# Performance work log

Hardware: AMD Instinct MI355X
Metric: run time of the kernel (lower is better)

## Reference

```python
import jax, jax.numpy as jnp
import numpy as np

N = 100000
E = 1600000
IN_DIM = 64
EMB_DIM = 64
BN_EPS = 1e-5


def setup_inputs() -> dict:
    key = jax.random.key(0)
    ks = jax.random.split(key, 8)
    x = jax.random.normal(ks[0], (N, IN_DIM), dtype=jnp.float32)
    edge_index = jax.random.randint(ks[1], (2, E), 0, N, dtype=jnp.int64)
    # GIN learned epsilon (train_eps=True), initialized to 0 as in PyG
    eps = jnp.zeros((), dtype=jnp.float32)
    # MLP params: Linear(in, emb) -> BN -> ReLU -> Linear(emb, emb)
    s1 = 1.0 / np.sqrt(IN_DIM)
    W1 = jax.random.uniform(ks[2], (IN_DIM, EMB_DIM), jnp.float32, -s1, s1)
    b1 = jax.random.uniform(ks[3], (EMB_DIM,), jnp.float32, -s1, s1)
    gamma = jnp.ones((EMB_DIM,), jnp.float32)
    beta = jnp.zeros((EMB_DIM,), jnp.float32)
    s2 = 1.0 / np.sqrt(EMB_DIM)
    W2 = jax.random.uniform(ks[4], (EMB_DIM, EMB_DIM), jnp.float32, -s2, s2)
    b2 = jax.random.uniform(ks[5], (EMB_DIM,), jnp.float32, -s2, s2)
    return {"x": x, "edge_index": edge_index, "eps": eps,
            "W1": W1, "b1": b1, "gamma": gamma, "beta": beta,
            "W2": W2, "b2": b2}


def reference(x, edge_index, eps, W1, b1, gamma, beta, W2, b2):
    src, dst = edge_index[0], edge_index[1]
    # GIN aggregation: sum of neighbor (source) features at each destination
    agg = jax.ops.segment_sum(x[src], dst, num_segments=N)  # [N, IN_DIM]
    h = (1.0 + eps) * x + agg
    # MLP: Linear -> BatchNorm1d (training-mode batch stats) -> ReLU -> Linear
    h1 = h @ W1 + b1                                   # [N, EMB_DIM]
    mean = jnp.mean(h1, axis=0)
    var = jnp.mean((h1 - mean) ** 2, axis=0)           # biased var, as torch BN
    h1n = (h1 - mean) * jax.lax.rsqrt(var + BN_EPS) * gamma + beta
    h2 = jax.nn.relu(h1n)
    return h2 @ W2 + b2                                # [N, EMB_DIM]
```

## Files before the change

### kernel.cpp

```cpp
#include <hip/hip_runtime.h>

#define NNODES 100000
#define NEDGES 1600000
#define DIM 64
#define NB 782
#define NPB 256
#define CHUNK 6250
#define CAP 3968
#define HP 68
#define NTILES 6250

typedef __attribute__((ext_vector_type(4))) float f32x4;
typedef __attribute__((ext_vector_type(8))) short s16x8;

__device__ __forceinline__ unsigned short bf16_rne(float f) {
  unsigned u = __float_as_uint(f);
  u += 0x7FFF + ((u >> 16) & 1);
  return (unsigned short)(u >> 16);
}
__device__ __forceinline__ float bf16_to_f32(unsigned short h) {
  return __uint_as_float(((unsigned)h) << 16);
}

__global__ __launch_bounds__(1024) void initpack_kernel(
    int* __restrict__ gcursor, float* __restrict__ sums,
    const float* __restrict__ W1, const float* __restrict__ W2,
    unsigned short* __restrict__ Wp1, unsigned short* __restrict__ Wp2) {
  int t = threadIdx.x;
  if (t < NB) gcursor[t] = t * CAP;
  if (t < 2 * DIM) sums[t] = 0.0f;
  if (t < 128) {
    int lane = t & 63;
    const float* W = (t >= 64) ? W2 : W1;
    unsigned short* Wp = (t >= 64) ? Wp2 : Wp1;
    int q = lane >> 4, n16 = lane & 15;
#pragma unroll
    for (int f = 0; f < 8; ++f) {
      int kk = f >> 2, nt = f & 3;
#pragma unroll
      for (int j = 0; j < 8; ++j) {
        int k = kk * 32 + q * 8 + j;
        int n = nt * 16 + n16;
        Wp[f * 512 + lane * 8 + j] = bf16_rne(W[k * DIM + n]);
      }
    }
  }
}

__global__ __launch_bounds__(256) void convert_kernel(
    const float* __restrict__ x, unsigned short* __restrict__ xb) {
  int i = blockIdx.x * 256 + threadIdx.x;
  float4 v = ((const float4*)x)[i];
  ushort4 o;
  o.x = bf16_rne(v.x); o.y = bf16_rne(v.y);
  o.z = bf16_rne(v.z); o.w = bf16_rne(v.w);
  ((ushort4*)xb)[i] = o;
}

__global__ __launch_bounds__(1024) void partition_kernel(
    const int* __restrict__ ei, int* __restrict__ gcursor,
    int* __restrict__ bpart) {
  __shared__ int lh[NB];
  __shared__ int cur[NB];
  int t = threadIdx.x;
  for (int b = t; b < NB; b += 1024) lh[b] = 0;
  __syncthreads();
  int base = blockIdx.x * CHUNK;
  for (int i = t; i < CHUNK; i += 1024)
    atomicAdd(&lh[ei[NEDGES + base + i] >> 7], 1);
  __syncthreads();
  for (int b = t; b < NB; b += 1024) {
    int c = lh[b];
    cur[b] = c ? atomicAdd(&gcursor[b], c) : 0;
  }
  __syncthreads();
  for (int i = t; i < CHUNK; i += 1024) {
    int s = ei[base + i];
    int d = ei[NEDGES + base + i];
    int p = atomicAdd(&cur[d >> 7], 1);
    bpart[p] = ((d & 127) << 17) | s;
  }
}

__global__ __launch_bounds__(512) void mega_kernel(
    const int* __restrict__ bpart, const int* __restrict__ gcursor,
    const unsigned short* __restrict__ xb, float* __restrict__ h1,
    const unsigned short* __restrict__ Wp, const float* __restrict__ b1,
    const float* __restrict__ epsp,
    float* __restrict__ sums, float* __restrict__ sumsq) {
  __shared__ int sd[128];
  __shared__ int cur[128];
  __shared__ int stage[CAP];
  __shared__ float hbuf[128 * HP];
  __shared__ float lsum[DIM];
  __shared__ float lsq[DIM];
  int b = blockIdx.x;
  int t = threadIdx.x;
  if (t < 128) sd[t] = 0;
  if (t < DIM) { lsum[t] = 0.0f; lsq[t] = 0.0f; }
  __syncthreads();
  int pbase = b * CAP;
  int cnt = gcursor[b] - pbase;
  for (int i = t; i < cnt; i += 512)
    atomicAdd(&sd[bpart[pbase + i] >> 17], 1);
  __syncthreads();
  int deg = (t < 128) ? sd[t] : 0;
  for (int off = 1; off < 128; off <<= 1) {
    int a = (t < 128 && t >= off) ? sd[t - off] : 0;
    __syncthreads();
    if (t < 128) sd[t] += a;
    __syncthreads();
  }
  if (t < 128) cur[t] = sd[t] - deg;
  __syncthreads();
  for (int i = t; i < cnt; i += 512) {
    int v = bpart[pbase + i];
    int p = atomicAdd(&cur[v >> 17], 1);
    stage[p] = v & 0x1FFFF;
  }
  __syncthreads();
  {
    int part = t & 15;
    int ng = t >> 4;
#pragma unroll 1
    for (int pass = 0; pass < 4; ++pass) {
      int nl = ng + pass * 32;
      int e0 = (nl == 0) ? 0 : sd[nl - 1];
      int e1 = sd[nl];
      float4 a0 = make_float4(0.f, 0.f, 0.f, 0.f);
      float4 a1 = a0, a2 = a0, a3 = a0;
      int e = e0;
      for (; e + 4 <= e1; e += 4) {
        int s0 = stage[e + 0];
        int s1 = stage[e + 1];
        int s2 = stage[e + 2];
        int s3 = stage[e + 3];
        ushort4 u0 = ((const ushort4*)(xb + (size_t)s0 * DIM))[part];
        ushort4 u1 = ((const ushort4*)(xb + (size_t)s1 * DIM))[part];
        ushort4 u2 = ((const ushort4*)(xb + (size_t)s2 * DIM))[part];
        ushort4 u3 = ((const ushort4*)(xb + (size_t)s3 * DIM))[part];
        a0.x += bf16_to_f32(u0.x); a0.y += bf16_to_f32(u0.y);
        a0.z += bf16_to_f32(u0.z); a0.w += bf16_to_f32(u0.w);
        a1.x += bf16_to_f32(u1.x); a1.y += bf16_to_f32(u1.y);
        a1.z += bf16_to_f32(u1.z); a1.w += bf16_to_f32(u1.w);
        a2.x += bf16_to_f32(u2.x); a2.y += bf16_to_f32(u2.y);
        a2.z += bf16_to_f32(u2.z); a2.w += bf16_to_f32(u2.w);
        a3.x += bf16_to_f32(u3.x); a3.y += bf16_to_f32(u3.y);
        a3.z += bf16_to_f32(u3.z); a3.w += bf16_to_f32(u3.w);
      }
      for (; e < e1; ++e) {
        int s = stage[e];
        ushort4 u = ((const ushort4*)(xb + (size_t)s * DIM))[part];
        a0.x += bf16_to_f32(u.x); a0.y += bf16_to_f32(u.y);
        a0.z += bf16_to_f32(u.z); a0.w += bf16_to_f32(u.w);
      }
      float4 acc;
      acc.x = (a0.x + a1.x) + (a2.x + a3.x);
      acc.y = (a0.y + a1.y) + (a2.y + a3.y);
      acc.z = (a0.z + a1.z) + (a2.z + a3.z);
      acc.w = (a0.w + a1.w) + (a2.w + a3.w);
      *(float4*)&hbuf[nl * HP + part * 4] = acc;
    }
  }
  __syncthreads();
  {
    int wave = t >> 6;
    int lane = t & 63;
    int tile = b * 8 + wave;
    if (tile < NTILES) {
      int q = lane >> 4;
      int r16 = lane & 15;
      float onep = 1.0f + epsp[0];
      s16x8 bf[8];
#pragma unroll
      for (int f = 0; f < 8; ++f)
        bf[f] = ((const s16x8*)Wp)[f * 64 + lane];
      int lrow = wave * 16 + r16;
      int grow = b * 128 + lrow;
      const s16x8* xrow = (const s16x8*)(xb + (size_t)grow * DIM);
      f32x4 acc[4] = {{0.f,0.f,0.f,0.f},{0.f,0.f,0.f,0.f},
                      {0.f,0.f,0.f,0.f},{0.f,0.f,0.f,0.f}};
#pragma unroll
      for (int kk = 0; kk < 2; ++kk) {
        s16x8 xv = xrow[kk * 4 + q];
        const float* hb = &hbuf[lrow * HP + kk * 32 + q * 8];
        float4 h0 = *(const float4*)hb;
        float4 h4 = *(const float4*)(hb + 4);
        s16x8 a;
        a[0] = (short)bf16_rne(fmaf(onep, bf16_to_f32((unsigned short)xv[0]), h0.x));
        a[1] = (short)bf16_rne(fmaf(onep, bf16_to_f32((unsigned short)xv[1]), h0.y));
        a[2] = (short)bf16_rne(fmaf(onep, bf16_to_f32((unsigned short)xv[2]), h0.z));
        a[3] = (short)bf16_rne(fmaf(onep, bf16_to_f32((unsigned short)xv[3]), h0.w));
        a[4] = (short)bf16_rne(fmaf(onep, bf16_to_f32((unsigned short)xv[4]), h4.x));
        a[5] = (short)bf16_rne(fmaf(onep, bf16_to_f32((unsigned short)xv[5]), h4.y));
        a[6] = (short)bf16_rne(fmaf(onep, bf16_to_f32((unsigned short)xv[6]), h4.z));
        a[7] = (short)bf16_rne(fmaf(onep, bf16_to_f32((unsigned short)xv[7]), h4.w));
#pragma unroll
        for (int nt = 0; nt < 4; ++nt)
          acc[nt] = __builtin_amdgcn_mfma_f32_16x16x32_bf16(
              a, bf[kk * 4 + nt], acc[nt], 0, 0, 0);
      }
      int orow = tile * 16 + q * 4;
#pragma unroll
      for (int nt = 0; nt < 4; ++nt) {
        int col = nt * 16 + r16;
        float bb = b1[col];
        float sl = 0.0f, ql = 0.0f;
#pragma unroll
        for (int r = 0; r < 4; ++r) {
          float v = acc[nt][r] + bb;
          h1[(size_t)(orow + r) * DIM + col] = v;
          sl += v;
          ql = fmaf(v, v, ql);
        }
        sl += __shfl_down(sl, 32); ql += __shfl_down(ql, 32);
        sl += __shfl_down(sl, 16); ql += __shfl_down(ql, 16);
        if (q == 0) {
          atomicAdd(&lsum[col], sl);
          atomicAdd(&lsq[col], ql);
        }
      }
    }
  }
  __syncthreads();
  if (t < DIM) {
    atomicAdd(&sums[t], lsum[t]);
    atomicAdd(&sumsq[t], lsq[t]);
  }
}

__global__ __launch_bounds__(256) void fused2_kernel(
    const float* __restrict__ h1, float* __restrict__ out,
    const unsigned short* __restrict__ Wp, const float* __restrict__ b2,
    const float* __restrict__ gamma, const float* __restrict__ beta,
    const float* __restrict__ sums, const float* __restrict__ sumsq) {
  __shared__ float sc_s[DIM];
  __shared__ float sh_s[DIM];
  int t = threadIdx.x;
  if (t < DIM) {
    float invN = 1.0f / (float)NNODES;
    float m = sums[t] * invN;
    float v = fmaf(-m, m, sumsq[t] * invN);
    float sc = gamma[t] * rsqrtf(v + 1e-5f);
    sc_s[t] = sc;
    sh_s[t] = fmaf(-m, sc, beta[t]);
  }
  __syncthreads();
  int wave = t >> 6;
  int lane = t & 63;
  int tile = blockIdx.x * 4 + wave;
  if (tile >= NTILES) return;
  int q = lane >> 4;
  int r16 = lane & 15;
  s16x8 bf[8];
#pragma unroll
  for (int f = 0; f < 8; ++f)
    bf[f] = ((const s16x8*)Wp)[f * 64 + lane];
  int arow = tile * 16 + r16;
  const float* hr = h1 + (size_t)arow * DIM + q * 8;
  f32x4 acc[4] = {{0.f,0.f,0.f,0.f},{0.f,0.f,0.f,0.f},
                  {0.f,0.f,0.f,0.f},{0.f,0.f,0.f,0.f}};
#pragma unroll
  for (int kk = 0; kk < 2; ++kk) {
    int kbase = kk * 32 + q * 8;
    float4 hv0 = *(const float4*)(hr + kk * 32);
    float4 hv1 = *(const float4*)(hr + kk * 32 + 4);
    float4 sc0 = *(const float4*)(sc_s + kbase);
    float4 sc1 = *(const float4*)(sc_s + kbase + 4);
    float4 sh0 = *(const float4*)(sh_s + kbase);
    float4 sh1 = *(const float4*)(sh_s + kbase + 4);
    s16x8 a;
    a[0] = (short)bf16_rne(fmaxf(fmaf(hv0.x, sc0.x, sh0.x), 0.f));
    a[1] = (short)bf16_rne(fmaxf(fmaf(hv0.y, sc0.y, sh0.y), 0.f));
    a[2] = (short)bf16_rne(fmaxf(fmaf(hv0.z, sc0.z, sh0.z), 0.f));
    a[3] = (short)bf16_rne(fmaxf(fmaf(hv0.w, sc0.w, sh0.w), 0.f));
    a[4] = (short)bf16_rne(fmaxf(fmaf(hv1.x, sc1.x, sh1.x), 0.f));
    a[5] = (short)bf16_rne(fmaxf(fmaf(hv1.y, sc1.y, sh1.y), 0.f));
    a[6] = (short)bf16_rne(fmaxf(fmaf(hv1.z, sc1.z, sh1.z), 0.f));
    a[7] = (short)bf16_rne(fmaxf(fmaf(hv1.w, sc1.w, sh1.w), 0.f));
#pragma unroll
    for (int nt = 0; nt < 4; ++nt)
      acc[nt] = __builtin_amdgcn_mfma_f32_16x16x32_bf16(
          a, bf[kk * 4 + nt], acc[nt], 0, 0, 0);
  }
  int orow = tile * 16 + q * 4;
#pragma unroll
  for (int nt = 0; nt < 4; ++nt) {
    int col = nt * 16 + r16;
    float bb = b2[col];
#pragma unroll
    for (int r = 0; r < 4; ++r)
      out[(size_t)(orow + r) * DIM + col] = acc[nt][r] + bb;
  }
}

extern "C" void kernel_launch(void* const* d_in, const int* in_sizes, int n_in,
                              void* d_out, int out_size, void* d_ws, size_t ws_size,
                              hipStream_t stream) {
  (void)in_sizes; (void)n_in; (void)out_size; (void)ws_size;
  const float* x     = (const float*)d_in[0];
  const int*   ei    = (const int*)d_in[1];
  const float* eps   = (const float*)d_in[2];
  const float* W1    = (const float*)d_in[3];
  const float* b1    = (const float*)d_in[4];
  const float* gamma = (const float*)d_in[5];
  const float* beta  = (const float*)d_in[6];
  const float* W2    = (const float*)d_in[7];
  const float* b2    = (const float*)d_in[8];
  float* outp = (float*)d_out;

  const int N = NNODES;

  float* h1      = (float*)d_ws;
  float* sums    = h1 + (size_t)N * DIM;
  float* sumsq   = sums + DIM;
  int*   gcursor = (int*)(sumsq + DIM);
  unsigned short* Wp1 = (unsigned short*)(gcursor + ((NB + 1) & ~1));
  unsigned short* Wp2 = Wp1 + 4096;
  int*            bpart = (int*)d_out;
  unsigned short* xb    = (unsigned short*)d_out + (size_t)NB * CAP * 2;

  initpack_kernel <<<1, 1024, 0, stream>>>(gcursor, sums, W1, W2, Wp1, Wp2);
  convert_kernel  <<<N * DIM / 4 / 256, 256, 0, stream>>>(x, xb);
  partition_kernel<<<NPB, 1024, 0, stream>>>(ei, gcursor, bpart);
  mega_kernel     <<<NB, 512, 0, stream>>>(bpart, gcursor, xb, h1,
                                           Wp1, b1, eps, sums, sumsq);
  fused2_kernel   <<<(NTILES + 3) / 4, 256, 0, stream>>>(h1, outp, Wp2, b2,
                                                         gamma, beta, sums, sumsq);
}
```

Measured before the change: 189.6 us.

## Merge init into convert kernel and stage partition output in shared memory for coalesced writes

Folds the single-block init/weight-pack kernel into the x-to-bf16 conversion kernel, removing one launch. The partition kernel now computes a block-wide prefix scan over bucket counts, sorts the edges of each chunk locally in shared memory, then writes them to global memory in contiguous runs per bucket. This replaces scattered per-edge global stores. In exchange it adds a 10-step scan with barriers and more shared memory per block.

```diff
diff --git a/kernel.cpp b/kernel.cpp
--- a/kernel.cpp
+++ b/kernel.cpp
@@ -22,64 +22,77 @@
   return __uint_as_float(((unsigned)h) << 16);
 }
 
-__global__ __launch_bounds__(1024) void initpack_kernel(
+__global__ __launch_bounds__(256) void prep_kernel(
+    const float* __restrict__ x, unsigned short* __restrict__ xb,
     int* __restrict__ gcursor, float* __restrict__ sums,
     const float* __restrict__ W1, const float* __restrict__ W2,
     unsigned short* __restrict__ Wp1, unsigned short* __restrict__ Wp2) {
-  int t = threadIdx.x;
-  if (t < NB) gcursor[t] = t * CAP;
-  if (t < 2 * DIM) sums[t] = 0.0f;
-  if (t < 128) {
-    int lane = t & 63;
-    const float* W = (t >= 64) ? W2 : W1;
-    unsigned short* Wp = (t >= 64) ? Wp2 : Wp1;
-    int q = lane >> 4, n16 = lane & 15;
-#pragma unroll
-    for (int f = 0; f < 8; ++f) {
-      int kk = f >> 2, nt = f & 3;
-#pragma unroll
-      for (int j = 0; j < 8; ++j) {
-        int k = kk * 32 + q * 8 + j;
-        int n = nt * 16 + n16;
-        Wp[f * 512 + lane * 8 + j] = bf16_rne(W[k * DIM + n]);
-      }
-    }
-  }
-}
-
-__global__ __launch_bounds__(256) void convert_kernel(
-    const float* __restrict__ x, unsigned short* __restrict__ xb) {
   int i = blockIdx.x * 256 + threadIdx.x;
   float4 v = ((const float4*)x)[i];
   ushort4 o;
   o.x = bf16_rne(v.x); o.y = bf16_rne(v.y);
   o.z = bf16_rne(v.z); o.w = bf16_rne(v.w);
   ((ushort4*)xb)[i] = o;
+  if (blockIdx.x == 0) {
+    int t = threadIdx.x;
+    for (int b = t; b < NB; b += 256) gcursor[b] = b * CAP;
+    if (t < 2 * DIM) sums[t] = 0.0f;
+    if (t < 128) {
+      int lane = t & 63;
+      const float* W = (t >= 64) ? W2 : W1;
+      unsigned short* Wp = (t >= 64) ? Wp2 : Wp1;
+      int q = lane >> 4, n16 = lane & 15;
+#pragma unroll
+      for (int f = 0; f < 8; ++f) {
+        int kk = f >> 2, nt = f & 3;
+#pragma unroll
+        for (int j = 0; j < 8; ++j) {
+          int k = kk * 32 + q * 8 + j;
+          int n = nt * 16 + n16;
+          Wp[f * 512 + lane * 8 + j] = bf16_rne(W[k * DIM + n]);
+        }
+      }
+    }
+  }
 }
 
 __global__ __launch_bounds__(1024) void partition_kernel(
     const int* __restrict__ ei, int* __restrict__ gcursor,
     int* __restrict__ bpart) {
-  __shared__ int lh[NB];
-  __shared__ int cur[NB];
+  __shared__ int sd[1024];
+  __shared__ int delta[1024];
+  __shared__ int lcur[1024];
+  __shared__ int stage[CHUNK];
+  __shared__ unsigned short sbuck[CHUNK];
   int t = threadIdx.x;
-  for (int b = t; b < NB; b += 1024) lh[b] = 0;
+  sd[t] = 0;
   __syncthreads();
   int base = blockIdx.x * CHUNK;
   for (int i = t; i < CHUNK; i += 1024)
-    atomicAdd(&lh[ei[NEDGES + base + i] >> 7], 1);
-  __syncthreads();
-  for (int b = t; b < NB; b += 1024) {
-    int c = lh[b];
-    cur[b] = c ? atomicAdd(&gcursor[b], c) : 0;
-  }
+    atomicAdd(&sd[ei[NEDGES + base + i] >> 7], 1);
+  __syncthreads();
+  int v = sd[t];
+  for (int off = 1; off < 1024; off <<= 1) {
+    int a = (t >= off) ? sd[t - off] : 0;
+    __syncthreads();
+    sd[t] += a;
+    __syncthreads();
+  }
+  int excl = sd[t] - v;
+  delta[t] = (v ? atomicAdd(&gcursor[t], v) : 0) - excl;
+  lcur[t] = excl;
   __syncthreads();
   for (int i = t; i < CHUNK; i += 1024) {
     int s = ei[base + i];
     int d = ei[NEDGES + base + i];
-    int p = atomicAdd(&cur[d >> 7], 1);
-    bpart[p] = ((d & 127) << 17) | s;
-  }
+    int b = d >> 7;
+    int p = atomicAdd(&lcur[b], 1);
+    stage[p] = ((d & 127) << 17) | s;
+    sbuck[p] = (unsigned short)b;
+  }
+  __syncthreads();
+  for (int i = t; i < CHUNK; i += 1024)
+    bpart[delta[sbuck[i]] + i] = stage[i];
 }
 
 __global__ __launch_bounds__(512) void mega_kernel(
@@ -320,8 +333,8 @@
   int*            bpart = (int*)d_out;
   unsigned short* xb    = (unsigned short*)d_out + (size_t)NB * CAP * 2;
 
-  initpack_kernel <<<1, 1024, 0, stream>>>(gcursor, sums, W1, W2, Wp1, Wp2);
-  convert_kernel  <<<N * DIM / 4 / 256, 256, 0, stream>>>(x, xb);
+  prep_kernel     <<<N * DIM / 4 / 256, 256, 0, stream>>>(x, xb, gcursor, sums,
+                                                          W1, W2, Wp1, Wp2);
   partition_kernel<<<NPB, 1024, 0, stream>>>(ei, gcursor, bpart);
   mega_kernel     <<<NB, 512, 0, stream>>>(bpart, gcursor, xb, h1,
                                            Wp1, b1, eps, sums, sumsq);
```

New measurement: 183.1 us. 1.04x faster.
